# Performance work log

Measured on AMD Instinct MI355X. Metric: run time of the kernel, lower is better.

Reference implementation:

```python
import jax, jax.numpy as jnp
import numpy as np

ROUTINGS = 3

def squash(s, axis=-1):
    mag_sq = jnp.sum(s * s, axis=axis, keepdims=True)
    mag = jnp.sqrt(mag_sq)
    return mag_sq / (1.0 + mag_sq) * (s / (mag + 1e-8))

def setup_inputs() -> dict:
    key = jax.random.key(0)
    k1, k2 = jax.random.split(key)
    B, I, Din, O, Dout = 256, 1152, 8, 10, 16
    x = jax.random.normal(k1, (B, I, Din), dtype=jnp.float32)
    weight = 0.01 * jax.random.normal(k2, (O, I, Dout, Din), dtype=jnp.float32)
    return {"x": x, "weight": weight}

def reference(x, weight):
    # x: [B, I, Din]; weight: [O, I, Dout, Din]
    # x_hat: [B, O, I, Dout]
    x_hat = jnp.einsum('oidc,bic->boid', weight, x)
    x_hat_det = jax.lax.stop_gradient(x_hat)
    B, O, I, _ = x_hat.shape
    b = jnp.zeros((B, O, I), dtype=x_hat.dtype)
    outputs = None
    for i in range(ROUTINGS):
        c = jax.nn.softmax(b, axis=1)  # softmax over output capsules
        if i == ROUTINGS - 1:
            outputs = squash(jnp.sum(c[:, :, :, None] * x_hat, axis=2, keepdims=True))
        else:
            outputs = squash(jnp.sum(c[:, :, :, None] * x_hat_det, axis=2, keepdims=True))
            b = b + jnp.sum(outputs * x_hat_det, axis=-1)
    return jnp.squeeze(outputs, axis=2)  # [B, O, Dout]
```

## Files before the change

kernel.cpp:

```cpp
#include <hip/hip_runtime.h>

#define BB   256
#define II   1152
#define OO   10
#define DOUT 16

using h2 = __fp16 __attribute__((ext_vector_type(2)));
using h4 = __fp16 __attribute__((ext_vector_type(4)));
using h8 = __fp16 __attribute__((ext_vector_type(8)));
#define H2V(v, a, b) __builtin_shufflevector((v), (v), (a), (b))
#define FD(a, b, c)  __builtin_amdgcn_fdot2((a), (b), (c), false)

__device__ __forceinline__ float dpp_add_xor1(float v) {
  int r = __builtin_amdgcn_mov_dpp(__float_as_int(v), 0xB1, 0xF, 0xF, true);
  return v + __int_as_float(r);
}
__device__ __forceinline__ float dpp_add_xor2(float v) {
  int r = __builtin_amdgcn_mov_dpp(__float_as_int(v), 0x4E, 0xF, 0xF, true);
  return v + __int_as_float(r);
}
__device__ __forceinline__ float swz_add_xor4(float v) {
  int r = __builtin_amdgcn_ds_swizzle(__float_as_int(v), 0x101F);
  return v + __int_as_float(r);
}

__device__ __forceinline__ void squash_pair(float v0, float v1,
                                            float& o0, float& o1) {
  float sq = v0 * v0 + v1 * v1;
  sq += __shfl_xor(sq, 1);
  sq += __shfl_xor(sq, 2);
  sq += __shfl_xor(sq, 4);
  const float mag = sqrtf(sq);
  const float t1  = sq / (1.f + sq);
  o0 = t1 * (v0 / (mag + 1e-8f));
  o1 = t1 * (v1 / (mag + 1e-8f));
}

__global__ __launch_bounds__(256) void convert_kernel(
    const float* __restrict__ x, const float* __restrict__ w,
    __fp16* __restrict__ x16, __fp16* __restrict__ w16)
{
  const int bid = blockIdx.x;
  if (bid < 2880) {
    const int t = bid * 256 + threadIdx.x;
    const int e = t & 63;
    const int r = t >> 6;
    const int o = r / II;
    const int i = r - o * II;
    const float2 v2 = *(const float2*)(w + (size_t)r * 128 + e * 2);
    *(h2*)(w16 + ((size_t)i * 12 + o) * 128 + e * 2) =
        __builtin_amdgcn_cvt_pkrtz(v2.x, v2.y);
  } else {
    const size_t t = (size_t)(bid - 2880) * 256 + threadIdx.x;
    const float4 v4 = *(const float4*)(x + t * 4);
    const h2 a = __builtin_amdgcn_cvt_pkrtz(v4.x, v4.y);
    const h2 c = __builtin_amdgcn_cvt_pkrtz(v4.z, v4.w);
    *(h4*)(x16 + t * 4) = __builtin_shufflevector(a, c, 0, 1, 2, 3);
  }
}

template<int K>
__global__ __launch_bounds__(256, 4) void pass_kernel(
    const __fp16* __restrict__ x16,
    const __fp16* __restrict__ w16,
    const float* __restrict__ r0,
    const float* __restrict__ r1,
    float* __restrict__ plane)
{
  const int tid  = threadIdx.x;
  const int lane = tid & 63;
  const int wv   = tid >> 6;
  const int dsub = lane & 7;
  const int bl   = lane >> 3;
  const int icg  = blockIdx.x & 31;
  const int bg   = blockIdx.x >> 5;
  const int b    = bg * 8 + bl;
  const int i0   = (icg * 4 + wv) * 9;

  __shared__ float red[4][8 * 168];

  float Vr[OO][2];
  if (K >= 1) {
#pragma unroll
    for (int o = 0; o < OO; ++o) {
      const float2 a = *(const float2*)(r0 + ((size_t)b * OO + o) * DOUT + dsub * 2);
      float v0, v1;
      squash_pair(a.x, a.y, v0, v1);
      if (K == 2) {
        const float2 c = *(const float2*)(r1 + ((size_t)b * OO + o) * DOUT + dsub * 2);
        float u0, u1;
        squash_pair(c.x, c.y, u0, u1);
        v0 += u0; v1 += u1;
      }
      Vr[o][0] = v0; Vr[o][1] = v1;
    }
  }

  float s[OO][2];
#pragma unroll
  for (int o = 0; o < OO; ++o) { s[o][0] = 0.f; s[o][1] = 0.f; }

  const __fp16* wp = w16 + (size_t)i0 * 1536 + dsub * 16;
  const __fp16* xp = x16 + ((size_t)b * II + i0) * 8;
  h8 xq = *(const h8*)(xp);
  h8 xn = *(const h8*)(xp + 8);

#pragma unroll 1
  for (int ii = 0; ii < 9; ++ii) {
    const h2 xq0 = H2V(xq, 0, 1), xq1 = H2V(xq, 2, 3);
    const h2 xq2 = H2V(xq, 4, 5), xq3 = H2V(xq, 6, 7);

    float xh[OO][2];
    float t[OO];
#pragma unroll
    for (int half = 0; half < 2; ++half) {
      h8 wz[10];
      const __fp16* base = wp + half * 640;
#pragma unroll
      for (int g = 0; g < 5; ++g) {
        wz[2 * g]     = *(const h8*)(base + g * 128);
        wz[2 * g + 1] = *(const h8*)(base + g * 128 + 8);
      }
      __builtin_amdgcn_sched_barrier(0);
#pragma unroll
      for (int g = 0; g < 5; ++g) {
        const int o = half * 5 + g;
        xh[o][0] = FD(H2V(wz[2*g], 0, 1), xq0, FD(H2V(wz[2*g], 2, 3), xq1,
                   FD(H2V(wz[2*g], 4, 5), xq2, FD(H2V(wz[2*g], 6, 7), xq3, 0.f))));
        xh[o][1] = FD(H2V(wz[2*g+1], 0, 1), xq0, FD(H2V(wz[2*g+1], 2, 3), xq1,
                   FD(H2V(wz[2*g+1], 4, 5), xq2, FD(H2V(wz[2*g+1], 6, 7), xq3, 0.f))));
        if (K >= 1)
          t[o] = Vr[o][0] * xh[o][0] + Vr[o][1] * xh[o][1];
      }
    }

    if (K == 0) {
#pragma unroll
      for (int o = 0; o < OO; ++o) { s[o][0] += xh[o][0]; s[o][1] += xh[o][1]; }
    } else {
#pragma unroll
      for (int o = 0; o < OO; ++o) {
        t[o] = dpp_add_xor1(t[o]);
        t[o] = dpp_add_xor2(t[o]);
        t[o] = swz_add_xor4(t[o]);
      }
      float sum = 0.f;
#pragma unroll
      for (int o = 0; o < OO; ++o) { t[o] = __expf(t[o]); sum += t[o]; }
      const float inv = __builtin_amdgcn_rcpf(sum);
#pragma unroll
      for (int o = 0; o < OO; ++o) {
        const float c = t[o] * inv;
        s[o][0] += c * xh[o][0];
        s[o][1] += c * xh[o][1];
      }
    }

    wp += 1536;
    xq = xn;
    const int inx = (ii < 7) ? (i0 + ii + 2) : (i0 + 8);
    xn = *(const h8*)(x16 + ((size_t)b * II + inx) * 8);
  }

  if (K == 0) {
#pragma unroll
    for (int o = 0; o < OO; ++o) { s[o][0] *= 0.1f; s[o][1] *= 0.1f; }
  }

  if (wv != 0) {
    float* rr = red[wv] + bl * 168;
#pragma unroll
    for (int o = 0; o < OO; ++o)
      *(float2*)&rr[o * 16 + dsub * 2] = make_float2(s[o][0], s[o][1]);
  }
  __syncthreads();
  if (wv == 0) {
    float* outp = plane + (size_t)b * (OO * DOUT);
#pragma unroll
    for (int o = 0; o < OO; ++o) {
      float a0 = s[o][0], a1 = s[o][1];
#pragma unroll
      for (int r = 1; r < 4; ++r) {
        const float2 v2 = *(const float2*)(red[r] + bl * 168 + o * 16 + dsub * 2);
        a0 += v2.x; a1 += v2.y;
      }
      unsafeAtomicAdd(&outp[o * 16 + dsub * 2],     a0);
      unsafeAtomicAdd(&outp[o * 16 + dsub * 2 + 1], a1);
    }
  }
}

__global__ __launch_bounds__(256) void final_kernel(
    const float* __restrict__ plane,
    float* __restrict__ out)
{
  const int idx = blockIdx.x * 256 + threadIdx.x;
  const float s = plane[idx];

  float sq = s * s;
  sq += __shfl_xor(sq, 1);
  sq += __shfl_xor(sq, 2);
  sq += __shfl_xor(sq, 4);
  sq += __shfl_xor(sq, 8);
  const float mag = sqrtf(sq);
  out[idx] = sq / (1.f + sq) * (s / (mag + 1e-8f));
}

extern "C" void kernel_launch(void* const* d_in, const int* in_sizes, int n_in,
                              void* d_out, int out_size, void* d_ws, size_t ws_size,
                              hipStream_t stream) {
  const float* x = (const float*)d_in[0];
  const float* w = (const float*)d_in[1];
  float* outp = (float*)d_out;

  const size_t P = (size_t)BB * OO * DOUT;
  float* s0 = (float*)d_ws;
  float* s1 = s0 + P;
  float* s2 = s1 + P;
  __fp16* x16 = (__fp16*)(s2 + P);
  __fp16* w16 = x16 + (size_t)BB * II * 8;

  hipMemsetAsync(s0, 0, 3 * P * sizeof(float), stream);
  convert_kernel<<<5184, 256, 0, stream>>>(x, w, x16, w16);

  const int pg = 1024;
  const int fg = (int)(P / 256);

  pass_kernel<0><<<pg, 256, 0, stream>>>(x16, w16, nullptr, nullptr, s0);
  pass_kernel<1><<<pg, 256, 0, stream>>>(x16, w16, s0, nullptr, s1);
  pass_kernel<2><<<pg, 256, 0, stream>>>(x16, w16, s0, s1, s2);
  final_kernel<<<fg, 256, 0, stream>>>(s2, outp);
}
```

Before: 163.9 us.

## Fuse routing passes into one persistent kernel with grid barriers

Replaces the three pass launches and the final squash launch with one kernel of 1024 blocks that runs all three routing phases, separated by a hierarchical atomic grid barrier, and then applies the final squash. This removes the gaps between kernel launches and the tail drain of each pass. It relies on all 1024 blocks being co-resident (4 blocks per CU from the launch bounds), otherwise the spin loop's timeout breaks the barrier early. It also switches to agent-scope atomic loads and safe atomicAdd for the cross-block partial sums.

```diff
diff --git a/kernel.cpp b/kernel.cpp
--- a/kernel.cpp
+++ b/kernel.cpp
@@ -4,6 +4,7 @@
 #define II   1152
 #define OO   10
 #define DOUT 16
+#define NBLK 1024
 
 using h2 = __fp16 __attribute__((ext_vector_type(2)));
 using h4 = __fp16 __attribute__((ext_vector_type(4)));
@@ -22,6 +23,10 @@
 __device__ __forceinline__ float swz_add_xor4(float v) {
   int r = __builtin_amdgcn_ds_swizzle(__float_as_int(v), 0x101F);
   return v + __int_as_float(r);
+}
+
+__device__ __forceinline__ float agent_ld(const float* p) {
+  return __hip_atomic_load(p, __ATOMIC_RELAXED, __HIP_MEMORY_SCOPE_AGENT);
 }
 
 __device__ __forceinline__ void squash_pair(float v0, float v1,
@@ -59,37 +64,46 @@
   }
 }
 
+__device__ __forceinline__ void grid_barrier(unsigned* sync, int p,
+                                             int tid, int bid) {
+  __syncthreads();
+  if (tid == 0) {
+    __threadfence();
+    unsigned* cnt    = sync + p * 256 + (bid & 7) * 16;
+    unsigned* master = sync + p * 256 + 128;
+    const unsigned a = __hip_atomic_fetch_add(cnt, 1, __ATOMIC_ACQ_REL,
+                                              __HIP_MEMORY_SCOPE_AGENT);
+    if (a + 1 == (NBLK / 8))
+      __hip_atomic_fetch_add(master, 1, __ATOMIC_ACQ_REL,
+                             __HIP_MEMORY_SCOPE_AGENT);
+    int spins = 0;
+    while (__hip_atomic_load(master, __ATOMIC_ACQUIRE,
+                             __HIP_MEMORY_SCOPE_AGENT) < 8u) {
+      __builtin_amdgcn_s_sleep(8);
+      if (++spins > (1 << 20)) break;
+    }
+  }
+  __syncthreads();
+}
+
 template<int K>
-__global__ __launch_bounds__(256, 4) void pass_kernel(
-    const __fp16* __restrict__ x16,
-    const __fp16* __restrict__ w16,
-    const float* __restrict__ r0,
-    const float* __restrict__ r1,
-    float* __restrict__ plane)
+__device__ __forceinline__ void phase(
+    const __fp16* __restrict__ x16, const __fp16* __restrict__ w16,
+    const float* __restrict__ r0, const float* __restrict__ r1,
+    float* __restrict__ plane, float (*red)[8 * 168],
+    const int wv, const int dsub, const int bl, const int b, const int i0)
 {
-  const int tid  = threadIdx.x;
-  const int lane = tid & 63;
-  const int wv   = tid >> 6;
-  const int dsub = lane & 7;
-  const int bl   = lane >> 3;
-  const int icg  = blockIdx.x & 31;
-  const int bg   = blockIdx.x >> 5;
-  const int b    = bg * 8 + bl;
-  const int i0   = (icg * 4 + wv) * 9;
-
-  __shared__ float red[4][8 * 168];
-
   float Vr[OO][2];
   if (K >= 1) {
 #pragma unroll
     for (int o = 0; o < OO; ++o) {
-      const float2 a = *(const float2*)(r0 + ((size_t)b * OO + o) * DOUT + dsub * 2);
+      const float* pp = r0 + ((size_t)b * OO + o) * DOUT + dsub * 2;
       float v0, v1;
-      squash_pair(a.x, a.y, v0, v1);
+      squash_pair(agent_ld(pp), agent_ld(pp + 1), v0, v1);
       if (K == 2) {
-        const float2 c = *(const float2*)(r1 + ((size_t)b * OO + o) * DOUT + dsub * 2);
+        const float* qq = r1 + ((size_t)b * OO + o) * DOUT + dsub * 2;
         float u0, u1;
-        squash_pair(c.x, c.y, u0, u1);
+        squash_pair(agent_ld(qq), agent_ld(qq + 1), u0, u1);
         v0 += u0; v1 += u1;
       }
       Vr[o][0] = v0; Vr[o][1] = v1;
@@ -184,26 +198,51 @@
         const float2 v2 = *(const float2*)(red[r] + bl * 168 + o * 16 + dsub * 2);
         a0 += v2.x; a1 += v2.y;
       }
-      unsafeAtomicAdd(&outp[o * 16 + dsub * 2],     a0);
-      unsafeAtomicAdd(&outp[o * 16 + dsub * 2 + 1], a1);
-    }
-  }
-}
-
-__global__ __launch_bounds__(256) void final_kernel(
-    const float* __restrict__ plane,
+      atomicAdd(&outp[o * 16 + dsub * 2],     a0);
+      atomicAdd(&outp[o * 16 + dsub * 2 + 1], a1);
+    }
+  }
+}
+
+__global__ __launch_bounds__(256, 4) void fused_kernel(
+    const __fp16* __restrict__ x16,
+    const __fp16* __restrict__ w16,
+    float* __restrict__ p0, float* __restrict__ p1, float* __restrict__ p2,
+    unsigned* __restrict__ sync,
     float* __restrict__ out)
 {
-  const int idx = blockIdx.x * 256 + threadIdx.x;
-  const float s = plane[idx];
-
-  float sq = s * s;
-  sq += __shfl_xor(sq, 1);
-  sq += __shfl_xor(sq, 2);
-  sq += __shfl_xor(sq, 4);
-  sq += __shfl_xor(sq, 8);
-  const float mag = sqrtf(sq);
-  out[idx] = sq / (1.f + sq) * (s / (mag + 1e-8f));
+  const int tid  = threadIdx.x;
+  const int bid  = blockIdx.x;
+  const int lane = tid & 63;
+  const int wv   = tid >> 6;
+  const int dsub = lane & 7;
+  const int bl   = lane >> 3;
+  const int icg  = bid & 31;
+  const int bg   = bid >> 5;
+  const int b    = bg * 8 + bl;
+  const int i0   = (icg * 4 + wv) * 9;
+
+  __shared__ float red[4][8 * 168];
+
+  phase<0>(x16, w16, nullptr, nullptr, p0, red, wv, dsub, bl, b, i0);
+  grid_barrier(sync, 0, tid, bid);
+
+  phase<1>(x16, w16, p0, nullptr, p1, red, wv, dsub, bl, b, i0);
+  grid_barrier(sync, 1, tid, bid);
+
+  phase<2>(x16, w16, p0, p1, p2, red, wv, dsub, bl, b, i0);
+  grid_barrier(sync, 2, tid, bid);
+
+  if (icg == 0 && wv == 0) {
+#pragma unroll
+    for (int o = 0; o < OO; ++o) {
+      const float* pp = p2 + ((size_t)b * OO + o) * DOUT + dsub * 2;
+      float u0, u1;
+      squash_pair(agent_ld(pp), agent_ld(pp + 1), u0, u1);
+      *(float2*)(out + ((size_t)b * OO + o) * DOUT + dsub * 2) =
+          make_float2(u0, u1);
+    }
+  }
 }
 
 extern "C" void kernel_launch(void* const* d_in, const int* in_sizes, int n_in,
@@ -217,17 +256,12 @@
   float* s0 = (float*)d_ws;
   float* s1 = s0 + P;
   float* s2 = s1 + P;
-  __fp16* x16 = (__fp16*)(s2 + P);
+  unsigned* sync = (unsigned*)(s2 + P);
+  __fp16* x16 = (__fp16*)(sync + 1024);
   __fp16* w16 = x16 + (size_t)BB * II * 8;
 
-  hipMemsetAsync(s0, 0, 3 * P * sizeof(float), stream);
+  hipMemsetAsync(s0, 0, 3 * P * sizeof(float) + 1024 * sizeof(unsigned), stream);
   convert_kernel<<<5184, 256, 0, stream>>>(x, w, x16, w16);
 
-  const int pg = 1024;
-  const int fg = (int)(P / 256);
-
-  pass_kernel<0><<<pg, 256, 0, stream>>>(x16, w16, nullptr, nullptr, s0);
-  pass_kernel<1><<<pg, 256, 0, stream>>>(x16, w16, s0, nullptr, s1);
-  pass_kernel<2><<<pg, 256, 0, stream>>>(x16, w16, s0, s1, s2);
-  final_kernel<<<fg, 256, 0, stream>>>(s2, outp);
-}
+  fused_kernel<<<NBLK, 256, 0, stream>>>(x16, w16, s0, s1, s2, sync, outp);
+}
```

After: 469.3 us. 186% more time.
